# Optimization experiments

Measured on AMD Instinct MI355X. Metric: run time of the kernel, lower is better.

## Reference

```python
import jax, jax.numpy as jnp
import numpy as np
from jax import lax

DIM = 256
HEADS = 8
P = 4  # split_size (patch_size)
SCALE = (DIM // HEADS) ** -0.5  # note: scale uses full head_dim = dim//heads, per the torch code


def _win(t, p1, p2, h):
    # 'b (h d) (gx p1) (gy p2) -> (b gx gy) h (p1 p2) d'
    b, c, X, Y = t.shape
    d = c // h
    gx, gy = X // p1, Y // p2
    t = t.reshape(b, h, d, gx, p1, gy, p2).transpose(0, 3, 5, 1, 4, 6, 2)
    return t.reshape(b * gx * gy, h, p1 * p2, d)


def _unwin(v, b, gx, gy, h, p1, p2):
    # '(b gx gy) h (p1 p2) d -> b (h d) (gx p1) (gy p2)'
    d = v.shape[-1]
    v = v.reshape(b, gx, gy, h, p1, p2, d).transpose(0, 3, 6, 1, 4, 2, 5)
    return v.reshape(b, h * d, gx * p1, gy * p2)


def _conv(x, w, stride):
    return lax.conv_general_dilated(x, w, stride, 'VALID',
                                    dimension_numbers=('NCHW', 'OIHW', 'NCHW'))


def _attn_branch(q, k, v, lepe):
    # q: (G,h,Nq,d), k/lepe: (G,h,Nk,d), v: (G,h,Nq,d)
    attn = jax.nn.softmax((q * SCALE) @ jnp.swapaxes(k, -2, -1), axis=-1)  # (G,h,Nq,Nk)
    # torch does attn.transpose(-2,-1) @ v + lepe -> output indexed by key tokens
    return jnp.einsum('ghqk,ghqd->ghkd', attn, v) + lepe


def setup_inputs() -> dict:
    key = jax.random.key(0)
    ks = jax.random.split(key, 6)
    b, x, y = 16, 64, 64
    fmap = jax.random.normal(ks[0], (b, DIM, x, y), dtype=jnp.float32)
    W_qvh = jax.random.normal(ks[1], (DIM, DIM // 2, 2, 1), dtype=jnp.float32) * 0.02
    W_qvv = jax.random.normal(ks[2], (DIM, DIM // 2, 1, 2), dtype=jnp.float32) * 0.02
    W_k = jax.random.normal(ks[3], (DIM, DIM), dtype=jnp.float32) * 0.02
    W_lepe = jax.random.normal(ks[4], (DIM, DIM), dtype=jnp.float32) * 0.02
    W_proj = jax.random.normal(ks[5], (DIM, DIM), dtype=jnp.float32) * 0.02
    return {"fmap": fmap, "W_qvh": W_qvh, "W_qvv": W_qvv,
            "W_k": W_k, "W_lepe": W_lepe, "W_proj": W_proj}


def reference(fmap, W_qvh, W_qvv, W_k, W_lepe, W_proj):
    b, n, x, y = fmap.shape
    h, p = HEADS, P
    half = n // 2
    # strided qv projections (size=0 path)
    qv_h = _conv(fmap[:, :half], W_qvh, (2, 1))  # (b, n, x/2, y)
    qv_v = _conv(fmap[:, half:], W_qvv, (1, 2))  # (b, n, x, y/2)
    # 1x1 convs as channel matmuls
    k_all = jnp.einsum('bcxy,oc->boxy', fmap, W_k)
    lepe_all = jnp.einsum('bcxy,oc->boxy', fmap, W_lepe)

    # horizontal branch: strips of width p spanning full height
    q_h = _win(qv_h[:, :half], x // 2, p, h)     # (b*(y/p), h, (x/2)*p, d)
    v_h = _win(qv_h[:, half:], x // 2, p, h)
    k_h = _win(k_all[:, :half], x, p, h)         # (b*(y/p), h, x*p, d)
    lepe_h = _win(lepe_all[:, :half], x, p, h)
    out_h = _attn_branch(q_h, k_h, v_h, lepe_h)  # (b*(y/p), h, x*p, d)
    out_h = _unwin(out_h, b, 1, y // p, h, x, p)  # (b, n/2, x, y)

    # vertical branch: strips of height p spanning full width
    q_v = _win(qv_v[:, :half], p, y // 2, h)
    v_v = _win(qv_v[:, half:], p, y // 2, h)
    k_v = _win(k_all[:, half:], p, y, h)
    lepe_v = _win(lepe_all[:, half:], p, y, h)
    out_v = _attn_branch(q_v, k_v, v_v, lepe_v)
    out_v = _unwin(out_v, b, x // p, 1, h, p, y)  # (b, n/2, x, y)

    cat = jnp.concatenate([out_h, out_v], axis=1)  # (b, n, x, y)
    return fmap + jnp.einsum('bcxy,oc->boxy', cat, W_proj)
```

## Files before the change

kernel.cpp:

```cpp
#include <hip/hip_runtime.h>
#include <hip/hip_bf16.h>

#define SCALE 0.1767766952966369f

typedef unsigned short bfu;
typedef unsigned int u32;
typedef __attribute__((ext_vector_type(8))) short bf8v;
typedef __attribute__((ext_vector_type(4))) float f32x4;
typedef __attribute__((ext_vector_type(8))) unsigned short u16x8;
typedef __attribute__((ext_vector_type(4))) unsigned int u32x4;

__device__ __forceinline__ bfu f2b(float x) {
    __hip_bfloat16 h = __float2bfloat16(x);
    return *(bfu*)&h;
}
__device__ __forceinline__ float bu2f(bfu u) {
    return __uint_as_float(((unsigned int)u) << 16);
}
__device__ __forceinline__ u32 cvtpk(float lo, float hi) {
    u32 r;
    asm("v_cvt_pk_bf16_f32 %0, %1, %2" : "=v"(r) : "v"(lo), "v"(hi));
    return r;
}
__device__ __forceinline__ void gload16(const bfu* g, bfu* l) {
    __builtin_amdgcn_global_load_lds(
        (const __attribute__((address_space(1))) unsigned int*)g,
        (__attribute__((address_space(3))) unsigned int*)l, 16, 0, 0);
}

__global__ __launch_bounds__(256) void k_prep_f(const float* __restrict__ fmap,
                                                bfu* __restrict__ Fbf) {
    const int x = blockIdx.x, b = blockIdx.y;
    const int t = threadIdx.x;
    __shared__ float tile[64][69];
    for (int cc = 0; cc < 256; cc += 64) {
        #pragma unroll
        for (int i = 0; i < 4; ++i) {
            const int c = (t >> 4) + i * 16, y4 = (t & 15) * 4;
            const float4 v = *(const float4*)(fmap + (((size_t)b * 256 + cc + c) * 64 + x) * 64 + y4);
            tile[y4][c] = v.x; tile[y4 + 1][c] = v.y; tile[y4 + 2][c] = v.z; tile[y4 + 3][c] = v.w;
        }
        __syncthreads();
        const int y = t >> 2, cs = (t & 3) * 16;
        u16x8 o0, o1;
        #pragma unroll
        for (int j = 0; j < 8; ++j) { o0[j] = f2b(tile[y][cs + j]); o1[j] = f2b(tile[y][cs + 8 + j]); }
        bfu* dst = Fbf + (((size_t)b * 64 + x) * 64 + y) * 256 + cc + cs;
        *(u16x8*)dst = o0; *(u16x8*)(dst + 8) = o1;
        __syncthreads();
    }
}

__global__ __launch_bounds__(256) void k_prep_w(
    const float* __restrict__ Wk, const float* __restrict__ Wl,
    const float* __restrict__ Wh, const float* __restrict__ Wv,
    bfu* __restrict__ Wkl, bfu* __restrict__ Whr, bfu* __restrict__ Wvr) {
    const int i = blockIdx.x * 256 + threadIdx.x;
    {
        const int o = i >> 8;
        Wkl[i] = f2b((o < 256) ? Wk[i] : Wl[i - 65536]);
    }
    if (i < 65536) {
        const int o = i >> 8, r = i & 255, kh = r >> 7, c = r & 127;
        const int s = (o * 128 + c) * 2 + kh;
        Whr[i] = f2b(Wh[s]);
        Wvr[i] = f2b(Wv[s]);
    }
}

template<int MODE>
__global__ __launch_bounds__(512) void k_gemm(
    const bfu* __restrict__ Ab16, const float* __restrict__ Af32,
    const bfu* __restrict__ Bsrc,
    bfu* __restrict__ o_kall, bfu* __restrict__ o_lepe, bfu* __restrict__ o_qv,
    const float* __restrict__ resid, float* __restrict__ outf) {
    const int nt = blockIdx.x, mt = blockIdx.y, b = blockIdx.z;
    const int n0 = nt * 128, m0 = mt * 128;
    const int t = threadIdx.x, lane = t & 63;
    const int wave = t >> 6;
    const int wm = wave >> 1, wn = wave & 1;
    const int lq = lane >> 4, lr = lane & 15;
    __shared__ bfu Bs[128 * 256];
    const bfu* fb = Bsrc + (size_t)b * 1048576;

    {
        const int lrow = lane >> 5;
        const int c1 = lane & 31;
        #pragma unroll
        for (int i = 0; i < 8; ++i) {
            const int row = wave * 16 + i * 2 + lrow;
            const int cS = c1 ^ (row & 7);
            int so;
            if (MODE == 0 || MODE == 3) {
                so = (n0 + row) * 256 + cS * 8;
            } else if (MODE == 1) {
                const int n = n0 + row;
                const int xo = n >> 6, y = n & 63;
                so = ((2 * xo + (cS >> 4)) * 64 + y) * 256 + (cS & 15) * 8;
            } else {
                const int n = n0 + row;
                const int x = n >> 5, yo = n & 31;
                so = (x * 64 + 2 * yo + (cS >> 4)) * 256 + 128 + (cS & 15) * 8;
            }
            gload16(fb + so, Bs + (wave * 16 + i * 2) * 256);
        }
    }
    __syncthreads();

    f32x4 acc[2][4];
    #pragma unroll
    for (int mi = 0; mi < 2; ++mi)
        #pragma unroll
        for (int ni = 0; ni < 4; ++ni) {
            acc[mi][ni][0] = 0.f; acc[mi][ni][1] = 0.f; acc[mi][ni][2] = 0.f; acc[mi][ni][3] = 0.f;
        }

    #pragma unroll
    for (int k0 = 0; k0 < 8; ++k0) {
        bf8v af[2], bv[4];
        if (MODE == 3) {
            #pragma unroll
            for (int mi = 0; mi < 2; ++mi) {
                const float* ap = Af32 + (size_t)(m0 + wm * 32 + mi * 16 + lr) * 256 + k0 * 32 + lq * 8;
                const float4 u0 = *(const float4*)ap;
                const float4 u1 = *(const float4*)(ap + 4);
                bf8v a;
                a[0] = (short)f2b(u0.x); a[1] = (short)f2b(u0.y);
                a[2] = (short)f2b(u0.z); a[3] = (short)f2b(u0.w);
                a[4] = (short)f2b(u1.x); a[5] = (short)f2b(u1.y);
                a[6] = (short)f2b(u1.z); a[7] = (short)f2b(u1.w);
                af[mi] = a;
            }
        } else {
            #pragma unroll
            for (int mi = 0; mi < 2; ++mi)
                af[mi] = *(const bf8v*)(Ab16 + (size_t)(m0 + wm * 32 + mi * 16 + lr) * 256 + k0 * 32 + lq * 8);
        }
        #pragma unroll
        for (int ni = 0; ni < 4; ++ni) {
            const int row = wn * 64 + ni * 16 + lr;
            const int ck = (k0 * 4 + lq) ^ (row & 7);
            bv[ni] = *(const bf8v*)(Bs + row * 256 + ck * 8);
        }
        #pragma unroll
        for (int mi = 0; mi < 2; ++mi)
            #pragma unroll
            for (int ni = 0; ni < 4; ++ni)
                acc[mi][ni] = __builtin_amdgcn_mfma_f32_16x16x32_bf16(af[mi], bv[ni], acc[mi][ni], 0, 0, 0);
    }

    if (MODE == 0) {
        bfu* outp = (mt < 2) ? o_kall : o_lepe;
        const int chb = (mt & 1) * 128 + wm * 32;
        #pragma unroll
        for (int mi = 0; mi < 2; ++mi)
            #pragma unroll
            for (int ni = 0; ni < 4; ++ni) {
                const int ch = chb + mi * 16 + lq * 4;
                const int ng = n0 + wn * 64 + ni * 16 + lr;
                ushort4 pk;
                pk.x = f2b(acc[mi][ni][0]); pk.y = f2b(acc[mi][ni][1]);
                pk.z = f2b(acc[mi][ni][2]); pk.w = f2b(acc[mi][ni][3]);
                *(ushort4*)(outp + ((size_t)b * 4096 + ng) * 256 + ch) = pk;
            }
    } else if (MODE == 1 || MODE == 2) {
        #pragma unroll
        for (int mi = 0; mi < 2; ++mi)
            #pragma unroll
            for (int ni = 0; ni < 4; ++ni) {
                const int ch = m0 + wm * 32 + mi * 16 + lq * 4;
                const int ng = n0 + wn * 64 + ni * 16 + lr;
                ushort4 pk;
                pk.x = f2b(acc[mi][ni][0]); pk.y = f2b(acc[mi][ni][1]);
                pk.z = f2b(acc[mi][ni][2]); pk.w = f2b(acc[mi][ni][3]);
                *(ushort4*)(o_qv + ((size_t)b * 2048 + ng) * 256 + ch) = pk;
            }
    } else {
        #pragma unroll
        for (int mi = 0; mi < 2; ++mi)
            #pragma unroll
            for (int ni = 0; ni < 4; ++ni) {
                const int ng = n0 + wn * 64 + ni * 16 + lr;
                #pragma unroll
                for (int r = 0; r < 4; ++r) {
                    const int m = m0 + wm * 32 + mi * 16 + lq * 4 + r;
                    const size_t ad = ((size_t)b * 256 + m) * 4096 + ng;
                    outf[ad] = resid[ad] + acc[mi][ni][r];
                }
            }
    }
}

template<int BR>
__global__ __launch_bounds__(256) void k_attn(
    const bfu* __restrict__ Qv, const bfu* __restrict__ Kb,
    const bfu* __restrict__ Lp, bfu* __restrict__ cat) {
    const int bid = blockIdx.x;
    const int h = (bid >> 8) & 7;
    const int bg = bid & 255;
    const int b = bg >> 4, g = bg & 15;
    const int t = threadIdx.x, lane = t & 63, w = t >> 6;
    const int lr = lane & 15, lq = lane >> 4;
    const int chQ = h * 16, chV = 128 + h * 16;
    const int chO = (BR == 0) ? h * 16 : 128 + h * 16;
    const bfu* Qb = Qv + (size_t)b * 2048 * 256;
    const bfu* Kg = Kb + (size_t)b * 4096 * 256 + chO;
    const bfu* Lg = Lp + (size_t)b * 4096 * 256 + chO;
    bfu* Cg = cat + (size_t)b * 4096 * 256 + chO;

    __shared__ __align__(16) bfu q_lds[128 * 16];
    __shared__ __align__(16) bfu v_lds[128 * 16];
    __shared__ float psum[2][256];

    {
        const int tok = (w << 5) + (lane >> 1), half = lane & 1;
        const int sp = (BR == 0) ? ((tok >> 2) * 64 + g * 4 + (tok & 3))
                                 : ((g * 4 + (tok >> 5)) * 32 + (tok & 31));
        gload16(Qb + (size_t)sp * 256 + chQ + half * 8, q_lds + w * 512);
        gload16(Qb + (size_t)sp * 256 + chV + half * 8, v_lds + w * 512);
    }

    bf8v kf[4];
    #pragma unroll
    for (int ct = 0; ct < 4; ++ct) {
        const int ktok = (4 * w + ct) * 16 + lr;
        const int sp = (BR == 0) ? ((ktok >> 2) * 64 + g * 4 + (ktok & 3))
                                 : ((g * 4 + (ktok >> 6)) * 64 + (ktok & 63));
        if (lq < 2) kf[ct] = *(const bf8v*)(Kg + (size_t)sp * 256 + lq * 8);
        else        kf[ct] = bf8v{0, 0, 0, 0, 0, 0, 0, 0};
    }
    __syncthreads();

    f32x4 oacc[4];
    #pragma unroll
    for (int ct = 0; ct < 4; ++ct) { oacc[ct][0] = 0.f; oacc[ct][1] = 0.f; oacc[ct][2] = 0.f; oacc[ct][3] = 0.f; }

    for (int gq = 0; gq < 2; ++gq) {
        bf8v qf[4];
        #pragma unroll
        for (int qt = 0; qt < 4; ++qt) {
            const int qtok = gq * 64 + qt * 16 + lr;
            if (lq < 2) qf[qt] = *(const bf8v*)(q_lds + qtok * 16 + lq * 8);
            else        qf[qt] = bf8v{0, 0, 0, 0, 0, 0, 0, 0};
        }
        bf8v vf[2];
        #pragma unroll
        for (int c = 0; c < 2; ++c)
            #pragma unroll
            for (int j = 0; j < 8; ++j)
                vf[c][j] = (short)v_lds[(gq * 64 + c * 32 + lq * 8 + j) * 16 + lr];

        f32x4 acc[4][4];
        #pragma unroll
        for (int qt = 0; qt < 4; ++qt)
            #pragma unroll
            for (int ct = 0; ct < 4; ++ct) {
                acc[qt][ct][0] = 0.f; acc[qt][ct][1] = 0.f; acc[qt][ct][2] = 0.f; acc[qt][ct][3] = 0.f;
            }
        #pragma unroll
        for (int qt = 0; qt < 4; ++qt)
            #pragma unroll
            for (int ct = 0; ct < 4; ++ct)
                acc[qt][ct] = __builtin_amdgcn_mfma_f32_16x16x32_bf16(qf[qt], kf[ct], acc[qt][ct], 0, 0, 0);

        #pragma unroll
        for (int qt = 0; qt < 4; ++qt)
            #pragma unroll
            for (int ct = 0; ct < 4; ++ct)
                #pragma unroll
                for (int r = 0; r < 4; ++r)
                    acc[qt][ct][r] = __expf(acc[qt][ct][r] * SCALE);

        float rr[4][4];
        #pragma unroll
        for (int qt = 0; qt < 4; ++qt)
            #pragma unroll
            for (int r = 0; r < 4; ++r)
                rr[qt][r] = (acc[qt][0][r] + acc[qt][1][r]) + (acc[qt][2][r] + acc[qt][3][r]);
        #pragma unroll
        for (int s = 1; s <= 8; s <<= 1)
            #pragma unroll
            for (int qt = 0; qt < 4; ++qt)
                #pragma unroll
                for (int r = 0; r < 4; ++r)
                    rr[qt][r] += __shfl_xor(rr[qt][r], s);
        if (lr == 0) {
            #pragma unroll
            for (int qt = 0; qt < 4; ++qt)
                #pragma unroll
                for (int r = 0; r < 4; ++r)
                    psum[gq][w * 64 + qt * 16 + lq * 4 + r] = rr[qt][r];
        }
        __syncthreads();
        float inv[4][4];
        #pragma unroll
        for (int qt = 0; qt < 4; ++qt)
            #pragma unroll
            for (int r = 0; r < 4; ++r) {
                const int qi = qt * 16 + lq * 4 + r;
                inv[qt][r] = 1.0f / ((psum[gq][qi] + psum[gq][64 + qi]) +
                                     (psum[gq][128 + qi] + psum[gq][192 + qi]));
            }

        u32 pk[4][4][2];
        #pragma unroll
        for (int qt = 0; qt < 4; ++qt)
            #pragma unroll
            for (int ct = 0; ct < 4; ++ct) {
                pk[qt][ct][0] = cvtpk(acc[qt][ct][0] * inv[qt][0], acc[qt][ct][1] * inv[qt][1]);
                pk[qt][ct][1] = cvtpk(acc[qt][ct][2] * inv[qt][2], acc[qt][ct][3] * inv[qt][3]);
            }

        const int base = ((lane >> 4) & 1) * 32 + (lane & 15);
        const bool hi = (lq >= 2);
        #pragma unroll
        for (int c = 0; c < 2; ++c) {
            #pragma unroll
            for (int ct = 0; ct < 4; ++ct) {
                const u32 a0 = (u32)__shfl((int)pk[2 * c][ct][0], base);
                const u32 a1 = (u32)__shfl((int)pk[2 * c][ct][1], base);
                const u32 a2 = (u32)__shfl((int)pk[2 * c][ct][0], base + 16);
                const u32 a3 = (u32)__shfl((int)pk[2 * c][ct][1], base + 16);
                const u32 b0 = (u32)__shfl((int)pk[2 * c + 1][ct][0], base);
                const u32 b1 = (u32)__shfl((int)pk[2 * c + 1][ct][1], base);
                const u32 b2 = (u32)__shfl((int)pk[2 * c + 1][ct][0], base + 16);
                const u32 b3 = (u32)__shfl((int)pk[2 * c + 1][ct][1], base + 16);
                u32x4 wd;
                wd[0] = hi ? b0 : a0; wd[1] = hi ? b1 : a1;
                wd[2] = hi ? b2 : a2; wd[3] = hi ? b3 : a3;
                const bf8v pf = __builtin_bit_cast(bf8v, wd);
                oacc[ct] = __builtin_amdgcn_mfma_f32_16x16x32_bf16(vf[c], pf, oacc[ct], 0, 0, 0);
            }
        }
    }

    #pragma unroll
    for (int ct = 0; ct < 4; ++ct) {
        const int ktok = (4 * w + ct) * 16 + lr;
        const int sp = (BR == 0) ? ((ktok >> 2) * 64 + g * 4 + (ktok & 3))
                                 : ((g * 4 + (ktok >> 6)) * 64 + (ktok & 63));
        const size_t off = (size_t)sp * 256 + lq * 4;
        const ushort4 l4 = *(const ushort4*)(Lg + off);
        ushort4 o;
        o.x = f2b(oacc[ct][0] + bu2f(l4.x));
        o.y = f2b(oacc[ct][1] + bu2f(l4.y));
        o.z = f2b(oacc[ct][2] + bu2f(l4.z));
        o.w = f2b(oacc[ct][3] + bu2f(l4.w));
        *(ushort4*)(Cg + off) = o;
    }
}

extern "C" void kernel_launch(void* const* d_in, const int* in_sizes, int n_in,
                              void* d_out, int out_size, void* d_ws, size_t ws_size,
                              hipStream_t stream) {
    const float* fmap = (const float*)d_in[0];
    const float* Wqvh = (const float*)d_in[1];
    const float* Wqvv = (const float*)d_in[2];
    const float* Wk   = (const float*)d_in[3];
    const float* Wl   = (const float*)d_in[4];
    const float* Wp   = (const float*)d_in[5];
    float* out = (float*)d_out;
    char* ws = (char*)d_ws;

    bfu* Fbf   = (bfu*)(ws);
    bfu* cat   = Fbf;
    bfu* k_all = (bfu*)(ws + 33554432);
    bfu* lepe  = (bfu*)(ws + 67108864);
    bfu* qvh   = (bfu*)(ws + 100663296);
    bfu* qvv   = (bfu*)(ws + 117440512);

    bfu* Wkl = (bfu*)d_out;
    bfu* Whr = (bfu*)((char*)d_out + 262144);
    bfu* Wvr = (bfu*)((char*)d_out + 393216);

    k_prep_f<<<dim3(64, 16), 256, 0, stream>>>(fmap, Fbf);
    k_prep_w<<<dim3(512), 256, 0, stream>>>(Wk, Wl, Wqvh, Wqvv, Wkl, Whr, Wvr);
    k_gemm<0><<<dim3(32, 4, 16), 512, 0, stream>>>(Wkl, nullptr, Fbf, k_all, lepe, nullptr, nullptr, nullptr);
    k_gemm<1><<<dim3(16, 2, 16), 512, 0, stream>>>(Whr, nullptr, Fbf, nullptr, nullptr, qvh, nullptr, nullptr);
    k_gemm<2><<<dim3(16, 2, 16), 512, 0, stream>>>(Wvr, nullptr, Fbf, nullptr, nullptr, qvv, nullptr, nullptr);
    k_attn<0><<<dim3(2048), 256, 0, stream>>>(qvh, k_all, lepe, cat);
    k_attn<1><<<dim3(2048), 256, 0, stream>>>(qvv, k_all, lepe, cat);
    k_gemm<3><<<dim3(32, 2, 16), 512, 0, stream>>>(nullptr, Wp, cat, nullptr, nullptr, nullptr, fmap, out);
}
```

Before: 251.3 us.

## Keep weights in registers and double-buffer activation tiles across four N tiles

The GEMM kernel now loads its A (weight) fragments once into registers and walks four 64-column N tiles per block. It double-buffers the LDS activation tile so the next tile's global load overlaps the current MFMA work, and halves the grid size. Separately, the softmax scale times log2(e) is folded into the Q projection epilogue, so the attention kernel can use exp2f without a multiply. This trades more registers per thread and fewer blocks for less redundant weight loading and better latency hiding.

Result: faster. 233.2 us (-7.2%).

```diff
diff --git a/kernel.cpp b/kernel.cpp
--- a/kernel.cpp
+++ b/kernel.cpp
@@ -1,7 +1,7 @@
 #include <hip/hip_runtime.h>
 #include <hip/hip_bf16.h>
 
-#define SCALE 0.1767766952966369f
+#define QSC 0.25503533f
 
 typedef unsigned short bfu;
 typedef unsigned int u32;
@@ -74,21 +74,45 @@
     const bfu* __restrict__ Bsrc,
     bfu* __restrict__ o_kall, bfu* __restrict__ o_lepe, bfu* __restrict__ o_qv,
     const float* __restrict__ resid, float* __restrict__ outf) {
-    const int nt = blockIdx.x, mt = blockIdx.y, b = blockIdx.z;
-    const int n0 = nt * 128, m0 = mt * 128;
+    const int ng = blockIdx.x, mt = blockIdx.y, b = blockIdx.z;
+    const int m0 = mt * 128;
     const int t = threadIdx.x, lane = t & 63;
     const int wave = t >> 6;
     const int wm = wave >> 1, wn = wave & 1;
     const int lq = lane >> 4, lr = lane & 15;
-    __shared__ bfu Bs[128 * 256];
+    __shared__ bfu Bs[2][64 * 256];
     const bfu* fb = Bsrc + (size_t)b * 1048576;
 
-    {
-        const int lrow = lane >> 5;
-        const int c1 = lane & 31;
-        #pragma unroll
-        for (int i = 0; i < 8; ++i) {
-            const int row = wave * 16 + i * 2 + lrow;
+    bf8v af[8][2];
+    if (MODE == 3) {
+        #pragma unroll
+        for (int k0 = 0; k0 < 8; ++k0)
+            #pragma unroll
+            for (int mi = 0; mi < 2; ++mi) {
+                const float* ap = Af32 + (size_t)(m0 + wm * 32 + mi * 16 + lr) * 256 + k0 * 32 + lq * 8;
+                const float4 u0 = *(const float4*)ap;
+                const float4 u1 = *(const float4*)(ap + 4);
+                bf8v a;
+                a[0] = (short)f2b(u0.x); a[1] = (short)f2b(u0.y);
+                a[2] = (short)f2b(u0.z); a[3] = (short)f2b(u0.w);
+                a[4] = (short)f2b(u1.x); a[5] = (short)f2b(u1.y);
+                a[6] = (short)f2b(u1.z); a[7] = (short)f2b(u1.w);
+                af[k0][mi] = a;
+            }
+    } else {
+        #pragma unroll
+        for (int k0 = 0; k0 < 8; ++k0)
+            #pragma unroll
+            for (int mi = 0; mi < 2; ++mi)
+                af[k0][mi] = *(const bf8v*)(Ab16 + (size_t)(m0 + wm * 32 + mi * 16 + lr) * 256 + k0 * 32 + lq * 8);
+    }
+
+    auto stage = [&](int buf, int nt) {
+        const int n0 = nt * 64;
+        const int lrow = lane >> 5, c1 = lane & 31;
+        #pragma unroll
+        for (int i = 0; i < 4; ++i) {
+            const int row = wave * 8 + i * 2 + lrow;
             const int cS = c1 ^ (row & 7);
             int so;
             if (MODE == 0 || MODE == 3) {
@@ -102,92 +126,85 @@
                 const int x = n >> 5, yo = n & 31;
                 so = (x * 64 + 2 * yo + (cS >> 4)) * 256 + 128 + (cS & 15) * 8;
             }
-            gload16(fb + so, Bs + (wave * 16 + i * 2) * 256);
-        }
-    }
+            gload16(fb + so, &Bs[buf][(wave * 8 + i * 2) * 256]);
+        }
+    };
+
+    const int nt0 = ng * 4;
+    stage(0, nt0);
     __syncthreads();
 
-    f32x4 acc[2][4];
-    #pragma unroll
-    for (int mi = 0; mi < 2; ++mi)
-        #pragma unroll
-        for (int ni = 0; ni < 4; ++ni) {
-            acc[mi][ni][0] = 0.f; acc[mi][ni][1] = 0.f; acc[mi][ni][2] = 0.f; acc[mi][ni][3] = 0.f;
-        }
-
-    #pragma unroll
-    for (int k0 = 0; k0 < 8; ++k0) {
-        bf8v af[2], bv[4];
-        if (MODE == 3) {
-            #pragma unroll
-            for (int mi = 0; mi < 2; ++mi) {
-                const float* ap = Af32 + (size_t)(m0 + wm * 32 + mi * 16 + lr) * 256 + k0 * 32 + lq * 8;
-                const float4 u0 = *(const float4*)ap;
-                const float4 u1 = *(const float4*)(ap + 4);
-                bf8v a;
-                a[0] = (short)f2b(u0.x); a[1] = (short)f2b(u0.y);
-                a[2] = (short)f2b(u0.z); a[3] = (short)f2b(u0.w);
-                a[4] = (short)f2b(u1.x); a[5] = (short)f2b(u1.y);
-                a[6] = (short)f2b(u1.z); a[7] = (short)f2b(u1.w);
-                af[mi] = a;
-            }
+    for (int tt = 0; tt < 4; ++tt) {
+        if (tt + 1 < 4) stage((tt + 1) & 1, nt0 + tt + 1);
+
+        const int buf = tt & 1;
+        f32x4 acc[2][2];
+        #pragma unroll
+        for (int mi = 0; mi < 2; ++mi)
+            #pragma unroll
+            for (int ni = 0; ni < 2; ++ni) {
+                acc[mi][ni][0] = 0.f; acc[mi][ni][1] = 0.f;
+                acc[mi][ni][2] = 0.f; acc[mi][ni][3] = 0.f;
+            }
+        #pragma unroll
+        for (int k0 = 0; k0 < 8; ++k0) {
+            bf8v bv[2];
+            #pragma unroll
+            for (int ni = 0; ni < 2; ++ni) {
+                const int row = wn * 32 + ni * 16 + lr;
+                const int ck = (k0 * 4 + lq) ^ (row & 7);
+                bv[ni] = *(const bf8v*)(&Bs[buf][row * 256 + ck * 8]);
+            }
+            #pragma unroll
+            for (int mi = 0; mi < 2; ++mi)
+                #pragma unroll
+                for (int ni = 0; ni < 2; ++ni)
+                    acc[mi][ni] = __builtin_amdgcn_mfma_f32_16x16x32_bf16(af[k0][mi], bv[ni], acc[mi][ni], 0, 0, 0);
+        }
+
+        const int n0 = (nt0 + tt) * 64;
+        if (MODE == 0) {
+            bfu* outp = (mt < 2) ? o_kall : o_lepe;
+            const int chb = (mt & 1) * 128 + wm * 32;
+            #pragma unroll
+            for (int mi = 0; mi < 2; ++mi)
+                #pragma unroll
+                for (int ni = 0; ni < 2; ++ni) {
+                    const int ch = chb + mi * 16 + lq * 4;
+                    const int ngl = n0 + wn * 32 + ni * 16 + lr;
+                    ushort4 pk;
+                    pk.x = f2b(acc[mi][ni][0]); pk.y = f2b(acc[mi][ni][1]);
+                    pk.z = f2b(acc[mi][ni][2]); pk.w = f2b(acc[mi][ni][3]);
+                    *(ushort4*)(outp + ((size_t)b * 4096 + ngl) * 256 + ch) = pk;
+                }
+        } else if (MODE == 1 || MODE == 2) {
+            const float qs = (mt == 0) ? QSC : 1.0f;
+            #pragma unroll
+            for (int mi = 0; mi < 2; ++mi)
+                #pragma unroll
+                for (int ni = 0; ni < 2; ++ni) {
+                    const int ch = m0 + wm * 32 + mi * 16 + lq * 4;
+                    const int ngl = n0 + wn * 32 + ni * 16 + lr;
+                    ushort4 pk;
+                    pk.x = f2b(acc[mi][ni][0] * qs); pk.y = f2b(acc[mi][ni][1] * qs);
+                    pk.z = f2b(acc[mi][ni][2] * qs); pk.w = f2b(acc[mi][ni][3] * qs);
+                    *(ushort4*)(o_qv + ((size_t)b * 2048 + ngl) * 256 + ch) = pk;
+                }
         } else {
             #pragma unroll
             for (int mi = 0; mi < 2; ++mi)
-                af[mi] = *(const bf8v*)(Ab16 + (size_t)(m0 + wm * 32 + mi * 16 + lr) * 256 + k0 * 32 + lq * 8);
-        }
-        #pragma unroll
-        for (int ni = 0; ni < 4; ++ni) {
-            const int row = wn * 64 + ni * 16 + lr;
-            const int ck = (k0 * 4 + lq) ^ (row & 7);
-            bv[ni] = *(const bf8v*)(Bs + row * 256 + ck * 8);
-        }
-        #pragma unroll
-        for (int mi = 0; mi < 2; ++mi)
-            #pragma unroll
-            for (int ni = 0; ni < 4; ++ni)
-                acc[mi][ni] = __builtin_amdgcn_mfma_f32_16x16x32_bf16(af[mi], bv[ni], acc[mi][ni], 0, 0, 0);
-    }
-
-    if (MODE == 0) {
-        bfu* outp = (mt < 2) ? o_kall : o_lepe;
-        const int chb = (mt & 1) * 128 + wm * 32;
-        #pragma unroll
-        for (int mi = 0; mi < 2; ++mi)
-            #pragma unroll
-            for (int ni = 0; ni < 4; ++ni) {
-                const int ch = chb + mi * 16 + lq * 4;
-                const int ng = n0 + wn * 64 + ni * 16 + lr;
-                ushort4 pk;
-                pk.x = f2b(acc[mi][ni][0]); pk.y = f2b(acc[mi][ni][1]);
-                pk.z = f2b(acc[mi][ni][2]); pk.w = f2b(acc[mi][ni][3]);
-                *(ushort4*)(outp + ((size_t)b * 4096 + ng) * 256 + ch) = pk;
-            }
-    } else if (MODE == 1 || MODE == 2) {
-        #pragma unroll
-        for (int mi = 0; mi < 2; ++mi)
-            #pragma unroll
-            for (int ni = 0; ni < 4; ++ni) {
-                const int ch = m0 + wm * 32 + mi * 16 + lq * 4;
-                const int ng = n0 + wn * 64 + ni * 16 + lr;
-                ushort4 pk;
-                pk.x = f2b(acc[mi][ni][0]); pk.y = f2b(acc[mi][ni][1]);
-                pk.z = f2b(acc[mi][ni][2]); pk.w = f2b(acc[mi][ni][3]);
-                *(ushort4*)(o_qv + ((size_t)b * 2048 + ng) * 256 + ch) = pk;
-            }
-    } else {
-        #pragma unroll
-        for (int mi = 0; mi < 2; ++mi)
-            #pragma unroll
-            for (int ni = 0; ni < 4; ++ni) {
-                const int ng = n0 + wn * 64 + ni * 16 + lr;
-                #pragma unroll
-                for (int r = 0; r < 4; ++r) {
-                    const int m = m0 + wm * 32 + mi * 16 + lq * 4 + r;
-                    const size_t ad = ((size_t)b * 256 + m) * 4096 + ng;
-                    outf[ad] = resid[ad] + acc[mi][ni][r];
+                #pragma unroll
+                for (int ni = 0; ni < 2; ++ni) {
+                    const int ngl = n0 + wn * 32 + ni * 16 + lr;
+                    #pragma unroll
+                    for (int r = 0; r < 4; ++r) {
+                        const int m = m0 + wm * 32 + mi * 16 + lq * 4 + r;
+                        const size_t ad = ((size_t)b * 256 + m) * 4096 + ngl;
+                        outf[ad] = resid[ad] + acc[mi][ni][r];
+                    }
                 }
-            }
+        }
+        if (tt + 1 < 4) __syncthreads();
     }
 }
 
@@ -269,7 +286,7 @@
             for (int ct = 0; ct < 4; ++ct)
                 #pragma unroll
                 for (int r = 0; r < 4; ++r)
-                    acc[qt][ct][r] = __expf(acc[qt][ct][r] * SCALE);
+                    acc[qt][ct][r] = exp2f(acc[qt][ct][r]);
 
         float rr[4][4];
         #pragma unroll
@@ -375,10 +392,10 @@
 
     k_prep_f<<<dim3(64, 16), 256, 0, stream>>>(fmap, Fbf);
     k_prep_w<<<dim3(512), 256, 0, stream>>>(Wk, Wl, Wqvh, Wqvv, Wkl, Whr, Wvr);
-    k_gemm<0><<<dim3(32, 4, 16), 512, 0, stream>>>(Wkl, nullptr, Fbf, k_all, lepe, nullptr, nullptr, nullptr);
-    k_gemm<1><<<dim3(16, 2, 16), 512, 0, stream>>>(Whr, nullptr, Fbf, nullptr, nullptr, qvh, nullptr, nullptr);
-    k_gemm<2><<<dim3(16, 2, 16), 512, 0, stream>>>(Wvr, nullptr, Fbf, nullptr, nullptr, qvv, nullptr, nullptr);
+    k_gemm<0><<<dim3(16, 4, 16), 512, 0, stream>>>(Wkl, nullptr, Fbf, k_all, lepe, nullptr, nullptr, nullptr);
+    k_gemm<1><<<dim3(8, 2, 16), 512, 0, stream>>>(Whr, nullptr, Fbf, nullptr, nullptr, qvh, nullptr, nullptr);
+    k_gemm<2><<<dim3(8, 2, 16), 512, 0, stream>>>(Wvr, nullptr, Fbf, nullptr, nullptr, qvv, nullptr, nullptr);
     k_attn<0><<<dim3(2048), 256, 0, stream>>>(qvh, k_all, lepe, cat);
     k_attn<1><<<dim3(2048), 256, 0, stream>>>(qvv, k_all, lepe, cat);
-    k_gemm<3><<<dim3(32, 2, 16), 512, 0, stream>>>(nullptr, Wp, cat, nullptr, nullptr, nullptr, fmap, out);
-}
+    k_gemm<3><<<dim3(16, 2, 16), 512, 0, stream>>>(nullptr, Wp, cat, nullptr, nullptr, nullptr, fmap, out);
+}
```
